# Performance work log

Hardware: AMD Instinct MI355X
Metric: run time of the kernel (lower is better)

Reference implementation:

```python
import jax, jax.numpy as jnp
import numpy as np

N_HEADS = 8

def setup_inputs() -> dict:
    key = jax.random.key(0)
    qkv = jax.random.normal(key, (4, 1, 3 * N_HEADS * 64, 2048), dtype=jnp.float32)
    return {"qkv": qkv}

def reference(qkv):
    # qkv: [N, G, 3*H*C, T]
    bs, groups, width, length = qkv.shape
    ch = width // (3 * N_HEADS)
    q, k, v = jnp.split(qkv, 3, axis=2)
    scale = 1.0 / np.sqrt(ch)  # applied to BOTH q and k (as in original)
    qr = (q * scale).reshape(bs, groups, N_HEADS, ch, length)
    kr = (k * scale).reshape(bs, groups, N_HEADS, ch, length)
    vr = v.reshape(bs, groups, N_HEADS, ch, length)
    weight = jnp.einsum('bghct,bghcs->bghts', qr, kr)  # [N,G,H,T,T]
    weight = jax.nn.softmax(weight.astype(jnp.float32), axis=-1).astype(qkv.dtype)
    a = jnp.einsum('bghts,bghcs->bghct', weight, vr)  # [N,G,H,C,T]
    return a.reshape(bs, -1, length)  # [N, G*H*C, T]
```

## Files before the change

### kernel.cpp

```cpp
#include <hip/hip_runtime.h>
#include <hip/hip_bf16.h>

typedef __attribute__((ext_vector_type(4))) float f32x4;
typedef __attribute__((ext_vector_type(16))) float f32x16;
typedef __attribute__((ext_vector_type(4))) float f4;
typedef __attribute__((ext_vector_type(8))) short bf16x8;
typedef __attribute__((ext_vector_type(4))) short s16x4;
typedef __attribute__((ext_vector_type(4))) unsigned u32x4;

#define T_LEN 2048
#define SPAD 72
#define QSCALE 0.022542110013890054f

#define SWZ(r) (((r) ^ ((r) >> 3)) & 7)

__device__ inline short f2bf(float f) {
  unsigned u = __builtin_bit_cast(unsigned, f);
  return (short)((u + 0x7fffu + ((u >> 16) & 1u)) >> 16);
}

__global__ __launch_bounds__(256) void prep(const float* __restrict__ qkv,
                                            short* __restrict__ kt,
                                            short* __restrict__ vb) {
  __shared__ float tile[64][65];
  const int bid = blockIdx.x;
  const int tid = threadIdx.x;

  if (bid < 1024) {
    const int tch = bid & 31;
    const int head = bid >> 5;
    const int b = head >> 3, h = head & 7;
    const float* src = qkv + ((size_t)b * 1536 + 512 + h * 64) * T_LEN + tch * 64;
    short* dst = kt + (size_t)head * 131072 + (size_t)tch * 4096;

    for (int e = tid; e < 4096; e += 256) {
      int c = e >> 6, t = e & 63;
      tile[c][t] = src[(size_t)c * T_LEN + t];
    }
    __syncthreads();
    for (int e = tid; e < 2048; e += 256) {
      int t = e >> 5, c2 = (e & 31) * 2;
      unsigned lo = (unsigned short)f2bf(tile[c2][t]);
      unsigned hi = (unsigned short)f2bf(tile[c2 + 1][t]);
      int cdst = c2 ^ (SWZ(t) << 3);
      *(unsigned*)&dst[t * 64 + cdst] = lo | (hi << 16);
    }
  } else {
    int id = (bid - 1024) * 256 + tid;
    int s4 = id & 15;
    int c = (id >> 4) & 63;
    int stile = (id >> 10) & 31;
    int head = id >> 15;
    int b = head >> 3, h = head & 7;
    const float* src =
        qkv + ((size_t)b * 1536 + 1024 + h * 64 + c) * T_LEN + stile * 64 + s4 * 4;
    f4 s = *(const f4*)src;
    s16x4 o;
#pragma unroll
    for (int j = 0; j < 4; ++j) o[j] = f2bf(s[j]);
    size_t dsts =
        (((size_t)head * 32 + stile) * 64 + c) * 64 + ((s4 * 4) ^ (SWZ(c) << 3));
    *(s16x4*)&vb[dsts] = o;
  }
}

__global__ __launch_bounds__(512, 4) void attn15(const float* __restrict__ qkv,
                                                 const short* __restrict__ Kt,
                                                 const short* __restrict__ Vb,
                                                 float* __restrict__ out) {
  __shared__ short KV[2][2][2][4096];

  const int bid = blockIdx.x;
  const int head = bid & 31;
  const int qblk = bid >> 5;

  const int tid = threadIdx.x;
  const int wave = tid >> 6;
  const int grp = wave >> 2;
  const int wv = wave & 3;
  const int lane = tid & 63;
  const int l31 = lane & 31;
  const int hi = lane >> 5;

  const int t0 = qblk * 128 + wv * 32;
  const int sbase = grp * 16;

  const int b = head >> 3, h = head & 7;
  const float* Qf = qkv + ((size_t)b * 1536 + h * 64) * T_LEN;
  const short* Kh = Kt + (size_t)head * 131072;
  const short* Vh = Vb + (size_t)head * 131072;
  float* O = out + (size_t)head * 131072;

  const int sw0 = SWZ(l31) << 3;
  const int sw1 = SWZ(l31 + 32) << 3;

  auto stage = [&](int buf, int it) {
#pragma unroll
    for (int j = 0; j < 4; ++j) {
      const int chunk = wv * 4 + j;
      const short* g =
          (chunk < 8 ? Kh : Vh) + (sbase + it) * 4096 + (chunk & 7) * 512 + lane * 8;
      short* l = &KV[grp][buf][chunk >> 3][(chunk & 7) * 512];
      __builtin_amdgcn_global_load_lds((const __attribute__((address_space(1))) void*)g,
                                       (__attribute__((address_space(3))) void*)l,
                                       16, 0, 0);
    }
  };

  stage(0, 0);

  bf16x8 aq[4];
#pragma unroll
  for (int ck = 0; ck < 4; ++ck) {
    float qv[8];
#pragma unroll
    for (int j = 0; j < 8; ++j)
      qv[j] = Qf[(size_t)(ck * 16 + hi * 8 + j) * T_LEN + t0 + l31];
#pragma unroll
    for (int j = 0; j < 8; ++j) aq[ck][j] = f2bf(qv[j] * QSCALE);
  }

  float l_lane = 0.f;
  f32x16 o_acc[2];
#pragma unroll
  for (int j = 0; j < 16; ++j) { o_acc[0][j] = 0.f; o_acc[1][j] = 0.f; }

  auto tile_body = [&](int buf) {
    f32x16 s0, s1;
#pragma unroll
    for (int j = 0; j < 16; ++j) { s0[j] = 0.f; s1[j] = 0.f; }
    __builtin_amdgcn_s_setprio(1);
#pragma unroll
    for (int ck = 0; ck < 4; ++ck) {
      const bf16x8 k0 = *(const bf16x8*)&KV[grp][buf][0][l31 * 64 + ((ck * 16 + hi * 8) ^ sw0)];
      s0 = __builtin_amdgcn_mfma_f32_32x32x16_bf16(k0, aq[ck], s0, 0, 0, 0);
      const bf16x8 k1 = *(const bf16x8*)&KV[grp][buf][0][(32 + l31) * 64 + ((ck * 16 + hi * 8) ^ sw1)];
      s1 = __builtin_amdgcn_mfma_f32_32x32x16_bf16(k1, aq[ck], s1, 0, 0, 0);
    }
    __builtin_amdgcn_s_setprio(0);

    float ps0 = 0.f, ps1 = 0.f, ps2 = 0.f, ps3 = 0.f;
    bf16x8 pf[4];
    const f32x16* sv[2] = {&s0, &s1};
#pragma unroll
    for (int sbk = 0; sbk < 2; ++sbk) {
      float p[16];
#pragma unroll
      for (int j = 0; j < 16; ++j) p[j] = __builtin_amdgcn_exp2f((*sv[sbk])[j]);
      ps0 += p[0] + p[4] + p[8] + p[12];
      ps1 += p[1] + p[5] + p[9] + p[13];
      ps2 += p[2] + p[6] + p[10] + p[14];
      ps3 += p[3] + p[7] + p[11] + p[15];
      unsigned w0, w1, w2, w3, w4, w5, w6, w7;
      asm("v_cvt_pk_bf16_f32 %0, %1, %2" : "=v"(w0) : "v"(p[0]), "v"(p[1]));
      asm("v_cvt_pk_bf16_f32 %0, %1, %2" : "=v"(w1) : "v"(p[2]), "v"(p[3]));
      asm("v_cvt_pk_bf16_f32 %0, %1, %2" : "=v"(w2) : "v"(p[4]), "v"(p[5]));
      asm("v_cvt_pk_bf16_f32 %0, %1, %2" : "=v"(w3) : "v"(p[6]), "v"(p[7]));
      asm("v_cvt_pk_bf16_f32 %0, %1, %2" : "=v"(w4) : "v"(p[8]), "v"(p[9]));
      asm("v_cvt_pk_bf16_f32 %0, %1, %2" : "=v"(w5) : "v"(p[10]), "v"(p[11]));
      asm("v_cvt_pk_bf16_f32 %0, %1, %2" : "=v"(w6) : "v"(p[12]), "v"(p[13]));
      asm("v_cvt_pk_bf16_f32 %0, %1, %2" : "=v"(w7) : "v"(p[14]), "v"(p[15]));
      asm("v_permlane32_swap_b32 %0, %1" : "+v"(w0), "+v"(w2));
      asm("v_permlane32_swap_b32 %0, %1" : "+v"(w1), "+v"(w3));
      asm("v_permlane32_swap_b32 %0, %1" : "+v"(w4), "+v"(w6));
      asm("v_permlane32_swap_b32 %0, %1" : "+v"(w5), "+v"(w7));
      u32x4 fe = {w0, w1, w2, w3};
      u32x4 fo = {w4, w5, w6, w7};
      pf[sbk * 2] = __builtin_bit_cast(bf16x8, fe);
      pf[sbk * 2 + 1] = __builtin_bit_cast(bf16x8, fo);
    }
    l_lane += (ps0 + ps1) + (ps2 + ps3);

    __builtin_amdgcn_s_setprio(1);
#pragma unroll
    for (int sc = 0; sc < 4; ++sc) {
      const bf16x8 v0 = *(const bf16x8*)&KV[grp][buf][1][l31 * 64 + ((sc * 16 + hi * 8) ^ sw0)];
      o_acc[0] = __builtin_amdgcn_mfma_f32_32x32x16_bf16(v0, pf[sc], o_acc[0], 0, 0, 0);
      const bf16x8 v1 = *(const bf16x8*)&KV[grp][buf][1][(32 + l31) * 64 + ((sc * 16 + hi * 8) ^ sw1)];
      o_acc[1] = __builtin_amdgcn_mfma_f32_32x32x16_bf16(v1, pf[sc], o_acc[1], 0, 0, 0);
    }
    __builtin_amdgcn_s_setprio(0);
  };

  __syncthreads();

  for (int itp = 0; itp < 8; ++itp) {
    const int it = itp * 2;
    stage(1, it + 1);
    tile_body(0);
    __syncthreads();
    if (itp < 7) stage(0, it + 2);
    tile_body(1);
    __syncthreads();
  }

  const float lg = l_lane + __shfl_xor(l_lane, 32, 64);
  float* xb = (float*)&KV[0][0][0][0];
  if (grp == 1) {
    float* dst = xb + (wv * 64 + lane) * 33;
#pragma unroll
    for (int j = 0; j < 16; ++j) { dst[j] = o_acc[0][j]; dst[16 + j] = o_acc[1][j]; }
    dst[32] = lg;
  }
  __syncthreads();
  if (grp == 0) {
    const float* src = xb + (wv * 64 + lane) * 33;
    const float rl = 1.0f / (lg + src[32]);
#pragma unroll
    for (int j = 0; j < 16; ++j) {
      const int c0 = (j & 3) + 8 * (j >> 2) + 4 * hi;
      O[(size_t)c0 * T_LEN + t0 + l31] = (o_acc[0][j] + src[j]) * rl;
      O[(size_t)(32 + c0) * T_LEN + t0 + l31] = (o_acc[1][j] + src[16 + j]) * rl;
    }
  }
}

__global__ __launch_bounds__(256) void attn_fwd(const float* __restrict__ qkv,
                                                float* __restrict__ out) {
  __shared__ short KtS[64][SPAD];
  __shared__ short VtS[64][SPAD];
  __shared__ short PbS[4][16][SPAD];

  const int bid = blockIdx.x;
  const int qt = bid & 31;
  const int head = bid >> 5;
  const int b = head >> 3, h = head & 7;

  const size_t base = ((size_t)b * 1536 + h * 64) * T_LEN;
  const float* Q = qkv + base;
  const float* K = qkv + base + (size_t)512 * T_LEN;
  const float* V = qkv + base + (size_t)1024 * T_LEN;
  float* O = out + ((size_t)b * 512 + h * 64) * T_LEN;

  const int tid = threadIdx.x;
  const int wave = tid >> 6;
  const int lane = tid & 63;
  const int l15 = lane & 15;
  const int l4 = lane >> 4;
  const int t0 = qt * 64 + wave * 16;

  bf16x8 aq[2];
#pragma unroll
  for (int kk = 0; kk < 2; ++kk)
#pragma unroll
    for (int j = 0; j < 8; ++j) {
      int c = kk * 32 + l4 * 8 + j;
      aq[kk][j] = f2bf(Q[(size_t)c * T_LEN + t0 + l15]);
    }

  float m_run[4], l_run[4];
  f32x4 o_acc[4];
#pragma unroll
  for (int r = 0; r < 4; ++r) { m_run[r] = -1e30f; l_run[r] = 0.f; }
#pragma unroll
  for (int n = 0; n < 4; ++n) o_acc[n] = (f32x4){0.f, 0.f, 0.f, 0.f};

  const float inv64 = 0.015625f;

  for (int s0 = 0; s0 < T_LEN; s0 += 64) {
    __syncthreads();
    for (int e = tid; e < 4096; e += 256) {
      int c = e >> 6, s = e & 63;
      KtS[s][c] = f2bf(K[(size_t)c * T_LEN + s0 + s]);
      VtS[c][s] = f2bf(V[(size_t)c * T_LEN + s0 + s]);
    }
    __syncthreads();

    f32x4 sacc[4];
#pragma unroll
    for (int n = 0; n < 4; ++n) {
      const bf16x8 bk0 = *(const bf16x8*)&KtS[16 * n + l15][l4 * 8];
      const bf16x8 bk1 = *(const bf16x8*)&KtS[16 * n + l15][32 + l4 * 8];
      f32x4 z = (f32x4){0.f, 0.f, 0.f, 0.f};
      z = __builtin_amdgcn_mfma_f32_16x16x32_bf16(aq[0], bk0, z, 0, 0, 0);
      z = __builtin_amdgcn_mfma_f32_16x16x32_bf16(aq[1], bk1, z, 0, 0, 0);
      sacc[n] = z;
    }

#pragma unroll
    for (int r = 0; r < 4; ++r) {
      float mx = fmaxf(fmaxf(sacc[0][r], sacc[1][r]),
                       fmaxf(sacc[2][r], sacc[3][r])) * inv64;
#pragma unroll
      for (int off = 8; off >= 1; off >>= 1)
        mx = fmaxf(mx, __shfl_xor(mx, off, 64));
      const float m_new = fmaxf(m_run[r], mx);
      const float alpha = __expf(m_run[r] - m_new);
      float psum = 0.f;
#pragma unroll
      for (int n = 0; n < 4; ++n) {
        float p = __expf(sacc[n][r] * inv64 - m_new);
        psum += p;
        PbS[wave][l4 * 4 + r][16 * n + l15] = f2bf(p);
      }
#pragma unroll
      for (int off = 8; off >= 1; off >>= 1)
        psum += __shfl_xor(psum, off, 64);
      l_run[r] = l_run[r] * alpha + psum;
      m_run[r] = m_new;
#pragma unroll
      for (int n = 0; n < 4; ++n) o_acc[n][r] *= alpha;
    }

    const bf16x8 ap0 = *(const bf16x8*)&PbS[wave][l15][l4 * 8];
    const bf16x8 ap1 = *(const bf16x8*)&PbS[wave][l15][32 + l4 * 8];
#pragma unroll
    for (int n = 0; n < 4; ++n) {
      const bf16x8 bv0 = *(const bf16x8*)&VtS[16 * n + l15][l4 * 8];
      const bf16x8 bv1 = *(const bf16x8*)&VtS[16 * n + l15][32 + l4 * 8];
      o_acc[n] = __builtin_amdgcn_mfma_f32_16x16x32_bf16(ap0, bv0, o_acc[n], 0, 0, 0);
      o_acc[n] = __builtin_amdgcn_mfma_f32_16x16x32_bf16(ap1, bv1, o_acc[n], 0, 0, 0);
    }
  }

#pragma unroll
  for (int n = 0; n < 4; ++n)
#pragma unroll
    for (int r = 0; r < 4; ++r) {
      const int c = 16 * n + l15;
      const int t = t0 + l4 * 4 + r;
      O[(size_t)c * T_LEN + t] = o_acc[n][r] / l_run[r];
    }
}

extern "C" void kernel_launch(void* const* d_in, const int* in_sizes, int n_in,
                              void* d_out, int out_size, void* d_ws, size_t ws_size,
                              hipStream_t stream) {
  const float* qkv = (const float*)d_in[0];
  float* out = (float*)d_out;
  const size_t per_buf = (size_t)32 * T_LEN * 64;
  const size_t need = per_buf * 2 * sizeof(short);
  if (ws_size >= need) {
    short* kt = (short*)d_ws;
    short* vb = kt + per_buf;
    hipLaunchKernelGGL(prep, dim3(5120), dim3(256), 0, stream, qkv, kt, vb);
    hipLaunchKernelGGL(attn15, dim3(512), dim3(512), 0, stream, qkv, kt, vb, out);
  } else {
    hipLaunchKernelGGL(attn_fwd, dim3(1024), dim3(256), 0, stream, qkv, out);
  }
}
```

Before: 53.75 us.

## Process two 32-row query tiles per wave to reuse K/V LDS fragments

Each wave now computes 64 query rows as two 32-row halves that share every K and V fragment loaded from LDS, doubling MFMA work per LDS read. The grid is halved and launch bounds relaxed to two blocks per CU to allow the extra accumulator registers. The epilogue merges the two key-split groups twice, once per half. The trade is lower occupancy and fewer blocks for better LDS reuse and amortised staging.

```diff
diff --git a/kernel.cpp b/kernel.cpp
--- a/kernel.cpp
+++ b/kernel.cpp
@@ -64,7 +64,7 @@
   }
 }
 
-__global__ __launch_bounds__(512, 4) void attn15(const float* __restrict__ qkv,
+__global__ __launch_bounds__(512, 2) void attn16(const float* __restrict__ qkv,
                                                  const short* __restrict__ Kt,
                                                  const short* __restrict__ Vb,
                                                  float* __restrict__ out) {
@@ -82,7 +82,7 @@
   const int l31 = lane & 31;
   const int hi = lane >> 5;
 
-  const int t0 = qblk * 128 + wv * 32;
+  const int t0 = qblk * 256 + wv * 64;
   const int sbase = grp * 16;
 
   const int b = head >> 3, h = head & 7;
@@ -109,38 +109,29 @@
 
   stage(0, 0);
 
-  bf16x8 aq[4];
+  bf16x8 aqA[4], aqB[4];
 #pragma unroll
   for (int ck = 0; ck < 4; ++ck) {
-    float qv[8];
-#pragma unroll
-    for (int j = 0; j < 8; ++j)
-      qv[j] = Qf[(size_t)(ck * 16 + hi * 8 + j) * T_LEN + t0 + l31];
-#pragma unroll
-    for (int j = 0; j < 8; ++j) aq[ck][j] = f2bf(qv[j] * QSCALE);
-  }
-
-  float l_lane = 0.f;
-  f32x16 o_acc[2];
-#pragma unroll
-  for (int j = 0; j < 16; ++j) { o_acc[0][j] = 0.f; o_acc[1][j] = 0.f; }
-
-  auto tile_body = [&](int buf) {
-    f32x16 s0, s1;
-#pragma unroll
-    for (int j = 0; j < 16; ++j) { s0[j] = 0.f; s1[j] = 0.f; }
-    __builtin_amdgcn_s_setprio(1);
-#pragma unroll
-    for (int ck = 0; ck < 4; ++ck) {
-      const bf16x8 k0 = *(const bf16x8*)&KV[grp][buf][0][l31 * 64 + ((ck * 16 + hi * 8) ^ sw0)];
-      s0 = __builtin_amdgcn_mfma_f32_32x32x16_bf16(k0, aq[ck], s0, 0, 0, 0);
-      const bf16x8 k1 = *(const bf16x8*)&KV[grp][buf][0][(32 + l31) * 64 + ((ck * 16 + hi * 8) ^ sw1)];
-      s1 = __builtin_amdgcn_mfma_f32_32x32x16_bf16(k1, aq[ck], s1, 0, 0, 0);
-    }
-    __builtin_amdgcn_s_setprio(0);
-
+    float qa[8], qb[8];
+#pragma unroll
+    for (int j = 0; j < 8; ++j) {
+      qa[j] = Qf[(size_t)(ck * 16 + hi * 8 + j) * T_LEN + t0 + l31];
+      qb[j] = Qf[(size_t)(ck * 16 + hi * 8 + j) * T_LEN + t0 + 32 + l31];
+    }
+#pragma unroll
+    for (int j = 0; j < 8; ++j) {
+      aqA[ck][j] = f2bf(qa[j] * QSCALE);
+      aqB[ck][j] = f2bf(qb[j] * QSCALE);
+    }
+  }
+
+  float lA = 0.f, lB = 0.f;
+  f32x16 oA0, oA1, oB0, oB1;
+#pragma unroll
+  for (int j = 0; j < 16; ++j) { oA0[j] = 0.f; oA1[j] = 0.f; oB0[j] = 0.f; oB1[j] = 0.f; }
+
+  auto pack = [&](const f32x16& s0, const f32x16& s1, bf16x8(&pf)[4], float& l_acc) {
     float ps0 = 0.f, ps1 = 0.f, ps2 = 0.f, ps3 = 0.f;
-    bf16x8 pf[4];
     const f32x16* sv[2] = {&s0, &s1};
 #pragma unroll
     for (int sbk = 0; sbk < 2; ++sbk) {
@@ -169,15 +160,38 @@
       pf[sbk * 2] = __builtin_bit_cast(bf16x8, fe);
       pf[sbk * 2 + 1] = __builtin_bit_cast(bf16x8, fo);
     }
-    l_lane += (ps0 + ps1) + (ps2 + ps3);
+    l_acc += (ps0 + ps1) + (ps2 + ps3);
+  };
+
+  auto tile_body = [&](int buf) {
+    f32x16 sA0, sA1, sB0, sB1;
+#pragma unroll
+    for (int j = 0; j < 16; ++j) { sA0[j] = 0.f; sA1[j] = 0.f; sB0[j] = 0.f; sB1[j] = 0.f; }
+    __builtin_amdgcn_s_setprio(1);
+#pragma unroll
+    for (int ck = 0; ck < 4; ++ck) {
+      const bf16x8 k0 = *(const bf16x8*)&KV[grp][buf][0][l31 * 64 + ((ck * 16 + hi * 8) ^ sw0)];
+      const bf16x8 k1 = *(const bf16x8*)&KV[grp][buf][0][(32 + l31) * 64 + ((ck * 16 + hi * 8) ^ sw1)];
+      sA0 = __builtin_amdgcn_mfma_f32_32x32x16_bf16(k0, aqA[ck], sA0, 0, 0, 0);
+      sA1 = __builtin_amdgcn_mfma_f32_32x32x16_bf16(k1, aqA[ck], sA1, 0, 0, 0);
+      sB0 = __builtin_amdgcn_mfma_f32_32x32x16_bf16(k0, aqB[ck], sB0, 0, 0, 0);
+      sB1 = __builtin_amdgcn_mfma_f32_32x32x16_bf16(k1, aqB[ck], sB1, 0, 0, 0);
+    }
+    __builtin_amdgcn_s_setprio(0);
+
+    bf16x8 pfA[4], pfB[4];
+    pack(sA0, sA1, pfA, lA);
+    pack(sB0, sB1, pfB, lB);
 
     __builtin_amdgcn_s_setprio(1);
 #pragma unroll
     for (int sc = 0; sc < 4; ++sc) {
       const bf16x8 v0 = *(const bf16x8*)&KV[grp][buf][1][l31 * 64 + ((sc * 16 + hi * 8) ^ sw0)];
-      o_acc[0] = __builtin_amdgcn_mfma_f32_32x32x16_bf16(v0, pf[sc], o_acc[0], 0, 0, 0);
       const bf16x8 v1 = *(const bf16x8*)&KV[grp][buf][1][(32 + l31) * 64 + ((sc * 16 + hi * 8) ^ sw1)];
-      o_acc[1] = __builtin_amdgcn_mfma_f32_32x32x16_bf16(v1, pf[sc], o_acc[1], 0, 0, 0);
+      oA0 = __builtin_amdgcn_mfma_f32_32x32x16_bf16(v0, pfA[sc], oA0, 0, 0, 0);
+      oA1 = __builtin_amdgcn_mfma_f32_32x32x16_bf16(v1, pfA[sc], oA1, 0, 0, 0);
+      oB0 = __builtin_amdgcn_mfma_f32_32x32x16_bf16(v0, pfB[sc], oB0, 0, 0, 0);
+      oB1 = __builtin_amdgcn_mfma_f32_32x32x16_bf16(v1, pfB[sc], oB1, 0, 0, 0);
     }
     __builtin_amdgcn_s_setprio(0);
   };
@@ -194,23 +208,44 @@
     __syncthreads();
   }
 
-  const float lg = l_lane + __shfl_xor(l_lane, 32, 64);
+  const float lAg = lA + __shfl_xor(lA, 32, 64);
+  const float lBg = lB + __shfl_xor(lB, 32, 64);
   float* xb = (float*)&KV[0][0][0][0];
+
   if (grp == 1) {
     float* dst = xb + (wv * 64 + lane) * 33;
 #pragma unroll
-    for (int j = 0; j < 16; ++j) { dst[j] = o_acc[0][j]; dst[16 + j] = o_acc[1][j]; }
-    dst[32] = lg;
+    for (int j = 0; j < 16; ++j) { dst[j] = oA0[j]; dst[16 + j] = oA1[j]; }
+    dst[32] = lAg;
   }
   __syncthreads();
   if (grp == 0) {
     const float* src = xb + (wv * 64 + lane) * 33;
-    const float rl = 1.0f / (lg + src[32]);
+    const float rl = 1.0f / (lAg + src[32]);
 #pragma unroll
     for (int j = 0; j < 16; ++j) {
       const int c0 = (j & 3) + 8 * (j >> 2) + 4 * hi;
-      O[(size_t)c0 * T_LEN + t0 + l31] = (o_acc[0][j] + src[j]) * rl;
-      O[(size_t)(32 + c0) * T_LEN + t0 + l31] = (o_acc[1][j] + src[16 + j]) * rl;
+      O[(size_t)c0 * T_LEN + t0 + l31] = (oA0[j] + src[j]) * rl;
+      O[(size_t)(32 + c0) * T_LEN + t0 + l31] = (oA1[j] + src[16 + j]) * rl;
+    }
+  }
+  __syncthreads();
+
+  if (grp == 1) {
+    float* dst = xb + (wv * 64 + lane) * 33;
+#pragma unroll
+    for (int j = 0; j < 16; ++j) { dst[j] = oB0[j]; dst[16 + j] = oB1[j]; }
+    dst[32] = lBg;
+  }
+  __syncthreads();
+  if (grp == 0) {
+    const float* src = xb + (wv * 64 + lane) * 33;
+    const float rl = 1.0f / (lBg + src[32]);
+#pragma unroll
+    for (int j = 0; j < 16; ++j) {
+      const int c0 = (j & 3) + 8 * (j >> 2) + 4 * hi;
+      O[(size_t)c0 * T_LEN + t0 + 32 + l31] = (oB0[j] + src[j]) * rl;
+      O[(size_t)(32 + c0) * T_LEN + t0 + 32 + l31] = (oB1[j] + src[16 + j]) * rl;
     }
   }
 }
@@ -334,7 +369,7 @@
     short* kt = (short*)d_ws;
     short* vb = kt + per_buf;
     hipLaunchKernelGGL(prep, dim3(5120), dim3(256), 0, stream, qkv, kt, vb);
-    hipLaunchKernelGGL(attn15, dim3(512), dim3(512), 0, stream, qkv, kt, vb, out);
+    hipLaunchKernelGGL(attn16, dim3(256), dim3(512), 0, stream, qkv, kt, vb, out);
   } else {
     hipLaunchKernelGGL(attn_fwd, dim3(1024), dim3(256), 0, stream, qkv, out);
   }
```

New measurement: 53.03 us. About the same (-1.3%).

## Split key range across separate blocks with partial outputs and a combine kernel

Applied to the files above, without the earlier changes.

Replaces the 512-thread attention kernel, in which two wave groups each covered half of the key sequence inside one block, with a 256-thread kernel launched on 1024 blocks, one per key half. Each block writes unnormalized partial outputs and row sums to global memory, and a new combine kernel adds the two halves and divides. The aim is finer-grained blocks with smaller LDS, for better occupancy and scheduling. The cost is an extra kernel launch plus a write and re-read of a full fp32 partial output buffer.

```diff
diff --git a/kernel.cpp b/kernel.cpp
--- a/kernel.cpp
+++ b/kernel.cpp
@@ -64,20 +64,21 @@
   }
 }
 
-__global__ __launch_bounds__(512, 4) void attn15(const float* __restrict__ qkv,
+__global__ __launch_bounds__(256, 4) void attn17(const float* __restrict__ qkv,
                                                  const short* __restrict__ Kt,
                                                  const short* __restrict__ Vb,
-                                                 float* __restrict__ out) {
-  __shared__ short KV[2][2][2][4096];
+                                                 float* __restrict__ po0,
+                                                 float* __restrict__ po1,
+                                                 float* __restrict__ lbuf) {
+  __shared__ short KV[2][2][4096];
 
   const int bid = blockIdx.x;
   const int head = bid & 31;
-  const int qblk = bid >> 5;
+  const int qblk = (bid >> 5) & 15;
+  const int grp = bid >> 9;
 
   const int tid = threadIdx.x;
-  const int wave = tid >> 6;
-  const int grp = wave >> 2;
-  const int wv = wave & 3;
+  const int wv = tid >> 6;
   const int lane = tid & 63;
   const int l31 = lane & 31;
   const int hi = lane >> 5;
@@ -89,7 +90,7 @@
   const float* Qf = qkv + ((size_t)b * 1536 + h * 64) * T_LEN;
   const short* Kh = Kt + (size_t)head * 131072;
   const short* Vh = Vb + (size_t)head * 131072;
-  float* O = out + (size_t)head * 131072;
+  float* PO = (grp ? po1 : po0) + (size_t)head * 131072;
 
   const int sw0 = SWZ(l31) << 3;
   const int sw1 = SWZ(l31 + 32) << 3;
@@ -100,7 +101,7 @@
       const int chunk = wv * 4 + j;
       const short* g =
           (chunk < 8 ? Kh : Vh) + (sbase + it) * 4096 + (chunk & 7) * 512 + lane * 8;
-      short* l = &KV[grp][buf][chunk >> 3][(chunk & 7) * 512];
+      short* l = &KV[buf][chunk >> 3][(chunk & 7) * 512];
       __builtin_amdgcn_global_load_lds((const __attribute__((address_space(1))) void*)g,
                                        (__attribute__((address_space(3))) void*)l,
                                        16, 0, 0);
@@ -132,9 +133,9 @@
     __builtin_amdgcn_s_setprio(1);
 #pragma unroll
     for (int ck = 0; ck < 4; ++ck) {
-      const bf16x8 k0 = *(const bf16x8*)&KV[grp][buf][0][l31 * 64 + ((ck * 16 + hi * 8) ^ sw0)];
+      const bf16x8 k0 = *(const bf16x8*)&KV[buf][0][l31 * 64 + ((ck * 16 + hi * 8) ^ sw0)];
       s0 = __builtin_amdgcn_mfma_f32_32x32x16_bf16(k0, aq[ck], s0, 0, 0, 0);
-      const bf16x8 k1 = *(const bf16x8*)&KV[grp][buf][0][(32 + l31) * 64 + ((ck * 16 + hi * 8) ^ sw1)];
+      const bf16x8 k1 = *(const bf16x8*)&KV[buf][0][(32 + l31) * 64 + ((ck * 16 + hi * 8) ^ sw1)];
       s1 = __builtin_amdgcn_mfma_f32_32x32x16_bf16(k1, aq[ck], s1, 0, 0, 0);
     }
     __builtin_amdgcn_s_setprio(0);
@@ -174,6 +175,163 @@
     __builtin_amdgcn_s_setprio(1);
 #pragma unroll
     for (int sc = 0; sc < 4; ++sc) {
+      const bf16x8 v0 = *(const bf16x8*)&KV[buf][1][l31 * 64 + ((sc * 16 + hi * 8) ^ sw0)];
+      o_acc[0] = __builtin_amdgcn_mfma_f32_32x32x16_bf16(v0, pf[sc], o_acc[0], 0, 0, 0);
+      const bf16x8 v1 = *(const bf16x8*)&KV[buf][1][(32 + l31) * 64 + ((sc * 16 + hi * 8) ^ sw1)];
+      o_acc[1] = __builtin_amdgcn_mfma_f32_32x32x16_bf16(v1, pf[sc], o_acc[1], 0, 0, 0);
+    }
+    __builtin_amdgcn_s_setprio(0);
+  };
+
+  __syncthreads();
+
+  for (int itp = 0; itp < 8; ++itp) {
+    const int it = itp * 2;
+    stage(1, it + 1);
+    tile_body(0);
+    __syncthreads();
+    if (itp < 7) stage(0, it + 2);
+    tile_body(1);
+    __syncthreads();
+  }
+
+  const float lg = l_lane + __shfl_xor(l_lane, 32, 64);
+  if (hi == 0)
+    lbuf[(size_t)grp * 65536 + head * 2048 + t0 + l31] = lg;
+#pragma unroll
+  for (int j = 0; j < 16; ++j) {
+    const int c0 = (j & 3) + 8 * (j >> 2) + 4 * hi;
+    PO[(size_t)c0 * T_LEN + t0 + l31] = o_acc[0][j];
+    PO[(size_t)(32 + c0) * T_LEN + t0 + l31] = o_acc[1][j];
+  }
+}
+
+__global__ __launch_bounds__(256) void combine(const float* __restrict__ po1,
+                                               const float* __restrict__ lbuf,
+                                               float* __restrict__ out) {
+  const size_t i = ((size_t)blockIdx.x * 256 + threadIdx.x) * 4;
+  const int head = (int)(i >> 17);
+  const int t = (int)(i & 2047);
+  f4 a = *(const f4*)&out[i];
+  f4 b2 = *(const f4*)&po1[i];
+  f4 l0 = *(const f4*)&lbuf[(size_t)head * 2048 + t];
+  f4 l1 = *(const f4*)&lbuf[65536 + (size_t)head * 2048 + t];
+  f4 r;
+#pragma unroll
+  for (int j = 0; j < 4; ++j) r[j] = (a[j] + b2[j]) / (l0[j] + l1[j]);
+  *(f4*)&out[i] = r;
+}
+
+__global__ __launch_bounds__(512, 4) void attn15(const float* __restrict__ qkv,
+                                                 const short* __restrict__ Kt,
+                                                 const short* __restrict__ Vb,
+                                                 float* __restrict__ out) {
+  __shared__ short KV[2][2][2][4096];
+
+  const int bid = blockIdx.x;
+  const int head = bid & 31;
+  const int qblk = bid >> 5;
+
+  const int tid = threadIdx.x;
+  const int wave = tid >> 6;
+  const int grp = wave >> 2;
+  const int wv = wave & 3;
+  const int lane = tid & 63;
+  const int l31 = lane & 31;
+  const int hi = lane >> 5;
+
+  const int t0 = qblk * 128 + wv * 32;
+  const int sbase = grp * 16;
+
+  const int b = head >> 3, h = head & 7;
+  const float* Qf = qkv + ((size_t)b * 1536 + h * 64) * T_LEN;
+  const short* Kh = Kt + (size_t)head * 131072;
+  const short* Vh = Vb + (size_t)head * 131072;
+  float* O = out + (size_t)head * 131072;
+
+  const int sw0 = SWZ(l31) << 3;
+  const int sw1 = SWZ(l31 + 32) << 3;
+
+  auto stage = [&](int buf, int it) {
+#pragma unroll
+    for (int j = 0; j < 4; ++j) {
+      const int chunk = wv * 4 + j;
+      const short* g =
+          (chunk < 8 ? Kh : Vh) + (sbase + it) * 4096 + (chunk & 7) * 512 + lane * 8;
+      short* l = &KV[grp][buf][chunk >> 3][(chunk & 7) * 512];
+      __builtin_amdgcn_global_load_lds((const __attribute__((address_space(1))) void*)g,
+                                       (__attribute__((address_space(3))) void*)l,
+                                       16, 0, 0);
+    }
+  };
+
+  stage(0, 0);
+
+  bf16x8 aq[4];
+#pragma unroll
+  for (int ck = 0; ck < 4; ++ck) {
+    float qv[8];
+#pragma unroll
+    for (int j = 0; j < 8; ++j)
+      qv[j] = Qf[(size_t)(ck * 16 + hi * 8 + j) * T_LEN + t0 + l31];
+#pragma unroll
+    for (int j = 0; j < 8; ++j) aq[ck][j] = f2bf(qv[j] * QSCALE);
+  }
+
+  float l_lane = 0.f;
+  f32x16 o_acc[2];
+#pragma unroll
+  for (int j = 0; j < 16; ++j) { o_acc[0][j] = 0.f; o_acc[1][j] = 0.f; }
+
+  auto tile_body = [&](int buf) {
+    f32x16 s0, s1;
+#pragma unroll
+    for (int j = 0; j < 16; ++j) { s0[j] = 0.f; s1[j] = 0.f; }
+    __builtin_amdgcn_s_setprio(1);
+#pragma unroll
+    for (int ck = 0; ck < 4; ++ck) {
+      const bf16x8 k0 = *(const bf16x8*)&KV[grp][buf][0][l31 * 64 + ((ck * 16 + hi * 8) ^ sw0)];
+      s0 = __builtin_amdgcn_mfma_f32_32x32x16_bf16(k0, aq[ck], s0, 0, 0, 0);
+      const bf16x8 k1 = *(const bf16x8*)&KV[grp][buf][0][(32 + l31) * 64 + ((ck * 16 + hi * 8) ^ sw1)];
+      s1 = __builtin_amdgcn_mfma_f32_32x32x16_bf16(k1, aq[ck], s1, 0, 0, 0);
+    }
+    __builtin_amdgcn_s_setprio(0);
+
+    float ps0 = 0.f, ps1 = 0.f, ps2 = 0.f, ps3 = 0.f;
+    bf16x8 pf[4];
+    const f32x16* sv[2] = {&s0, &s1};
+#pragma unroll
+    for (int sbk = 0; sbk < 2; ++sbk) {
+      float p[16];
+#pragma unroll
+      for (int j = 0; j < 16; ++j) p[j] = __builtin_amdgcn_exp2f((*sv[sbk])[j]);
+      ps0 += p[0] + p[4] + p[8] + p[12];
+      ps1 += p[1] + p[5] + p[9] + p[13];
+      ps2 += p[2] + p[6] + p[10] + p[14];
+      ps3 += p[3] + p[7] + p[11] + p[15];
+      unsigned w0, w1, w2, w3, w4, w5, w6, w7;
+      asm("v_cvt_pk_bf16_f32 %0, %1, %2" : "=v"(w0) : "v"(p[0]), "v"(p[1]));
+      asm("v_cvt_pk_bf16_f32 %0, %1, %2" : "=v"(w1) : "v"(p[2]), "v"(p[3]));
+      asm("v_cvt_pk_bf16_f32 %0, %1, %2" : "=v"(w2) : "v"(p[4]), "v"(p[5]));
+      asm("v_cvt_pk_bf16_f32 %0, %1, %2" : "=v"(w3) : "v"(p[6]), "v"(p[7]));
+      asm("v_cvt_pk_bf16_f32 %0, %1, %2" : "=v"(w4) : "v"(p[8]), "v"(p[9]));
+      asm("v_cvt_pk_bf16_f32 %0, %1, %2" : "=v"(w5) : "v"(p[10]), "v"(p[11]));
+      asm("v_cvt_pk_bf16_f32 %0, %1, %2" : "=v"(w6) : "v"(p[12]), "v"(p[13]));
+      asm("v_cvt_pk_bf16_f32 %0, %1, %2" : "=v"(w7) : "v"(p[14]), "v"(p[15]));
+      asm("v_permlane32_swap_b32 %0, %1" : "+v"(w0), "+v"(w2));
+      asm("v_permlane32_swap_b32 %0, %1" : "+v"(w1), "+v"(w3));
+      asm("v_permlane32_swap_b32 %0, %1" : "+v"(w4), "+v"(w6));
+      asm("v_permlane32_swap_b32 %0, %1" : "+v"(w5), "+v"(w7));
+      u32x4 fe = {w0, w1, w2, w3};
+      u32x4 fo = {w4, w5, w6, w7};
+      pf[sbk * 2] = __builtin_bit_cast(bf16x8, fe);
+      pf[sbk * 2 + 1] = __builtin_bit_cast(bf16x8, fo);
+    }
+    l_lane += (ps0 + ps1) + (ps2 + ps3);
+
+    __builtin_amdgcn_s_setprio(1);
+#pragma unroll
+    for (int sc = 0; sc < 4; ++sc) {
       const bf16x8 v0 = *(const bf16x8*)&KV[grp][buf][1][l31 * 64 + ((sc * 16 + hi * 8) ^ sw0)];
       o_acc[0] = __builtin_amdgcn_mfma_f32_32x32x16_bf16(v0, pf[sc], o_acc[0], 0, 0, 0);
       const bf16x8 v1 = *(const bf16x8*)&KV[grp][buf][1][(32 + l31) * 64 + ((sc * 16 + hi * 8) ^ sw1)];
@@ -329,8 +487,18 @@
   const float* qkv = (const float*)d_in[0];
   float* out = (float*)d_out;
   const size_t per_buf = (size_t)32 * T_LEN * 64;
-  const size_t need = per_buf * 2 * sizeof(short);
-  if (ws_size >= need) {
+  const size_t need_kv = per_buf * 2 * sizeof(short);
+  const size_t need_split = need_kv + per_buf * sizeof(float) + 131072 * sizeof(float);
+  if (ws_size >= need_split) {
+    short* kt = (short*)d_ws;
+    short* vb = kt + per_buf;
+    float* po1 = (float*)(vb + per_buf);
+    float* lbuf = po1 + per_buf;
+    hipLaunchKernelGGL(prep, dim3(5120), dim3(256), 0, stream, qkv, kt, vb);
+    hipLaunchKernelGGL(attn17, dim3(1024), dim3(256), 0, stream, qkv, kt, vb,
+                       out, po1, lbuf);
+    hipLaunchKernelGGL(combine, dim3(4096), dim3(256), 0, stream, po1, lbuf, out);
+  } else if (ws_size >= need_kv) {
     short* kt = (short*)d_ws;
     short* vb = kt + per_buf;
     hipLaunchKernelGGL(prep, dim3(5120), dim3(256), 0, stream, qkv, kt, vb);
```

Measured after the change: 64.28 us. 1.2x slower.
